# Kernel optimization log

Measured on AMD Instinct MI355X. Metric: run time of the kernel, lower is better.

The kernel has to match this reference:

```python
import jax, jax.numpy as jnp
import numpy as np

RGB2GRAY = jnp.array([0.299, 0.587, 0.114], dtype=jnp.float32)

H_IMG, W_IMG = 1080, 1920
NUM, GRID_Y, GRID_X, GRID_W = 1, 16, 16, 8


def _identity_grids(num, grid_y, grid_x, grid_w):
    ident = jnp.array([1., 0, 0, 0, 0, 1., 0, 0, 0, 0, 1., 0], dtype=jnp.float32)
    return jnp.broadcast_to(ident, (num, grid_y, grid_x, grid_w, 12))


def setup_inputs() -> dict:
    key = jax.random.key(0)
    k1, k2 = jax.random.split(key)
    rgb = jax.random.uniform(k1, (3, H_IMG, W_IMG), dtype=jnp.float32)
    # learned grids = identity affine + small perturbation (so slicing is non-trivial)
    grids = _identity_grids(NUM, GRID_Y, GRID_X, GRID_W) \
        + 0.05 * jax.random.normal(k2, (NUM, GRID_Y, GRID_X, GRID_W, 12), dtype=jnp.float32)
    return {"rgb": rgb, "grids": grids, "idx": 0}


def _bilateral_slice(grid, guidance):
    """Trilinear slice. grid: (Hg, Wg, L, 12); guidance: (Hi, Wi) in [0,1].
    Returns (Hi, Wi, 12)."""
    Hg, Wg, L, _ = grid.shape
    Hi, Wi = guidance.shape
    # align_corners-style pixel -> grid coords
    gy = jnp.linspace(0.0, Hg - 1.0, Hi, dtype=jnp.float32)[:, None]   # (Hi,1)
    gx = jnp.linspace(0.0, Wg - 1.0, Wi, dtype=jnp.float32)[None, :]   # (1,Wi)
    gz = jnp.clip(guidance, 0.0, 1.0) * (L - 1.0)                      # (Hi,Wi)

    fy = jnp.floor(gy); wy = gy - fy
    fx = jnp.floor(gx); wx = gx - fx
    fz = jnp.floor(gz); wz = gz - fz
    y0 = jnp.clip(fy.astype(jnp.int32), 0, Hg - 1); y1 = jnp.clip(y0 + 1, 0, Hg - 1)
    x0 = jnp.clip(fx.astype(jnp.int32), 0, Wg - 1); x1 = jnp.clip(x0 + 1, 0, Wg - 1)
    z0 = jnp.clip(fz.astype(jnp.int32), 0, L - 1);  z1 = jnp.clip(z0 + 1, 0, L - 1)

    out = jnp.zeros((Hi, Wi, 12), dtype=grid.dtype)
    for yi, wyi in ((y0, 1.0 - wy), (y1, wy)):
        for xi, wxi in ((x0, 1.0 - wx), (x1, wx)):
            for zi, wzi in ((z0, 1.0 - wz), (z1, wz)):
                w = (wyi * wxi * wzi)[..., None]          # (Hi,Wi,1)
                out = out + grid[yi, xi, zi] * w          # gather -> (Hi,Wi,12)
    return out


def reference(rgb, grids, idx):
    grid = grids[idx]                         # (Hg, Wg, L, 12)
    rgb_hwc = jnp.transpose(rgb, (1, 2, 0))   # (H, W, 3)
    gray = jnp.tensordot(rgb_hwc, RGB2GRAY, axes=([-1], [0]))  # (H, W)
    affine = _bilateral_slice(grid, gray)     # (H, W, 12)
    affine_mat = affine.reshape(-1, 3, 4)     # (H*W, 3, 4)
    rgb_flat = rgb_hwc.reshape(-1, 3)         # (H*W, 3)
    res_rgb = jnp.einsum('nij,nj->ni', affine_mat[..., :3], rgb_flat) + affine_mat[..., 3]
    return (affine_mat, res_rgb)
```

## Files before the change

kernel.cpp:

```cpp
#include <hip/hip_runtime.h>

#define H_IMG 1080
#define W_IMG 1920
#define HW_PIX (H_IMG * W_IMG)
#define GY 16
#define GX 16
#define GL 8
#define CF 12
#define SEG 192

__global__ __launch_bounds__(192) void bg_kernel(
    const float* __restrict__ rgb,
    const float* __restrict__ grids,
    const int* __restrict__ idxp,
    float* __restrict__ out)
{
    __shared__ float4 sg[96];

    const int tid = threadIdx.x;
    const int y = blockIdx.y;
    const int xbase = blockIdx.x * SEG;

    const float* grid = grids + (size_t)idxp[0] * (GY * GX * GL * CF);

    float gyv = (float)y * (15.0f / 1079.0f);
    float fy = floorf(gyv);
    float wy = gyv - fy;
    int y0 = min(max((int)fy, 0), GY - 1);
    int y1 = min(y0 + 1, GY - 1);

    int xc0 = (int)floorf((float)xbase * (15.0f / 1919.0f));

    if (tid < 96) {
        int xi  = tid / 24;
        int rem = tid - xi * 24;
        int z   = rem / 3;
        int c4  = rem - z * 3;
        int xc  = min(xc0 + xi, GX - 1);
        const float4* c0 = (const float4*)(grid + (size_t)((y0 * GX + xc) * GL + z) * CF) + c4;
        const float4* c1 = (const float4*)(grid + (size_t)((y1 * GX + xc) * GL + z) * CF) + c4;
        float4 a = *c0, b = *c1;
        float wy0 = 1.0f - wy;
        float4 r;
        r.x = wy0 * a.x + wy * b.x;
        r.y = wy0 * a.y + wy * b.y;
        r.z = wy0 * a.z + wy * b.z;
        r.w = wy0 * a.w + wy * b.w;
        sg[tid] = r;
    }
    __syncthreads();

    const int x = xbase + tid;
    const int p = y * W_IMG + x;

    float r = rgb[p];
    float g = rgb[HW_PIX + p];
    float b = rgb[2 * HW_PIX + p];

    float gray = 0.299f * r + 0.587f * g + 0.114f * b;

    float gxv = (float)x * (15.0f / 1919.0f);
    float fx = floorf(gxv), wx = gxv - fx;
    float gz = fminf(fmaxf(gray, 0.0f), 1.0f) * 7.0f;
    float fz = floorf(gz), wz = gz - fz;

    int x0g = min(max((int)fx, 0), GX - 1);
    int x1g = min(x0g + 1, GX - 1);
    int xi0 = x0g - xc0;
    int xi1 = x1g - xc0;
    int z0 = min(max((int)fz, 0), GL - 1);
    int z1 = min(z0 + 1, GL - 1);

    float w00 = (1.0f - wx) * (1.0f - wz);
    float w01 = (1.0f - wx) * wz;
    float w10 = wx * (1.0f - wz);
    float w11 = wx * wz;

    const float4* A = sg + (xi0 * 24 + z0 * 3);
    const float4* B = sg + (xi0 * 24 + z1 * 3);
    const float4* C = sg + (xi1 * 24 + z0 * 3);
    const float4* D = sg + (xi1 * 24 + z1 * 3);

    float4 acc[3];
#pragma unroll
    for (int j = 0; j < 3; ++j) {
        float4 va = A[j], vb = B[j], vc = C[j], vd = D[j];
        float4 o;
        o.x = fmaf(w00, va.x, fmaf(w01, vb.x, fmaf(w10, vc.x, w11 * vd.x)));
        o.y = fmaf(w00, va.y, fmaf(w01, vb.y, fmaf(w10, vc.y, w11 * vd.y)));
        o.z = fmaf(w00, va.z, fmaf(w01, vb.z, fmaf(w10, vc.z, w11 * vd.z)));
        o.w = fmaf(w00, va.w, fmaf(w01, vb.w, fmaf(w10, vc.w, w11 * vd.w)));
        acc[j] = o;
    }

    float4* ao = (float4*)out + (size_t)p * 3;
    ao[0] = acc[0];
    ao[1] = acc[1];
    ao[2] = acc[2];

    float res0 = fmaf(acc[0].x, r, fmaf(acc[0].y, g, fmaf(acc[0].z, b, acc[0].w)));
    float res1 = fmaf(acc[1].x, r, fmaf(acc[1].y, g, fmaf(acc[1].z, b, acc[1].w)));
    float res2 = fmaf(acc[2].x, r, fmaf(acc[2].y, g, fmaf(acc[2].z, b, acc[2].w)));

    float* ro = out + (size_t)HW_PIX * 12 + (size_t)p * 3;
    ro[0] = res0;
    ro[1] = res1;
    ro[2] = res2;
}

extern "C" void kernel_launch(void* const* d_in, const int* in_sizes, int n_in,
                              void* d_out, int out_size, void* d_ws, size_t ws_size,
                              hipStream_t stream) {
    const float* rgb   = (const float*)d_in[0];
    const float* grids = (const float*)d_in[1];
    const int*   idx   = (const int*)d_in[2];
    float*       out   = (float*)d_out;

    dim3 grid(W_IMG / SEG, H_IMG);
    dim3 block(SEG);
    bg_kernel<<<grid, block, 0, stream>>>(rgb, grids, idx, out);
}
```

Before: 154.0 us.

## Assign three threads per pixel so output stores are fully coalesced

Each pixel's work is now split across three threads, one per affine row, with blocks of 128 pixels (384 threads). Consecutive threads write consecutive float4s and consecutive floats, so the stores for both the affine and result outputs become contiguous instead of strided by 3. The trade-off is that the rgb loads and the gray and weight computation are repeated three times per pixel. The shared grid slice also shrinks to three x-cells.

```diff
diff --git a/kernel.cpp b/kernel.cpp
--- a/kernel.cpp
+++ b/kernel.cpp
@@ -7,19 +7,20 @@
 #define GX 16
 #define GL 8
 #define CF 12
-#define SEG 192
+#define PPB 128
+#define TPB (PPB * 3)
 
-__global__ __launch_bounds__(192) void bg_kernel(
+__global__ __launch_bounds__(TPB) void bg_kernel(
     const float* __restrict__ rgb,
     const float* __restrict__ grids,
     const int* __restrict__ idxp,
     float* __restrict__ out)
 {
-    __shared__ float4 sg[96];
+    __shared__ float4 sg[72];
 
     const int tid = threadIdx.x;
     const int y = blockIdx.y;
-    const int xbase = blockIdx.x * SEG;
+    const int xbase = blockIdx.x * PPB;
 
     const float* grid = grids + (size_t)idxp[0] * (GY * GX * GL * CF);
 
@@ -31,7 +32,7 @@
 
     int xc0 = (int)floorf((float)xbase * (15.0f / 1919.0f));
 
-    if (tid < 96) {
+    if (tid < 72) {
         int xi  = tid / 24;
         int rem = tid - xi * 24;
         int z   = rem / 3;
@@ -41,16 +42,18 @@
         const float4* c1 = (const float4*)(grid + (size_t)((y1 * GX + xc) * GL + z) * CF) + c4;
         float4 a = *c0, b = *c1;
         float wy0 = 1.0f - wy;
-        float4 r;
-        r.x = wy0 * a.x + wy * b.x;
-        r.y = wy0 * a.y + wy * b.y;
-        r.z = wy0 * a.z + wy * b.z;
-        r.w = wy0 * a.w + wy * b.w;
-        sg[tid] = r;
+        float4 rr;
+        rr.x = wy0 * a.x + wy * b.x;
+        rr.y = wy0 * a.y + wy * b.y;
+        rr.z = wy0 * a.z + wy * b.z;
+        rr.w = wy0 * a.w + wy * b.w;
+        sg[tid] = rr;
     }
     __syncthreads();
 
-    const int x = xbase + tid;
+    const int k = tid / 3;
+    const int c = tid - k * 3;
+    const int x = xbase + k;
     const int p = y * W_IMG + x;
 
     float r = rgb[p];
@@ -76,36 +79,23 @@
     float w10 = wx * (1.0f - wz);
     float w11 = wx * wz;
 
-    const float4* A = sg + (xi0 * 24 + z0 * 3);
-    const float4* B = sg + (xi0 * 24 + z1 * 3);
-    const float4* C = sg + (xi1 * 24 + z0 * 3);
-    const float4* D = sg + (xi1 * 24 + z1 * 3);
+    float4 A = sg[(xi0 * GL + z0) * 3 + c];
+    float4 B = sg[(xi0 * GL + z1) * 3 + c];
+    float4 C = sg[(xi1 * GL + z0) * 3 + c];
+    float4 D = sg[(xi1 * GL + z1) * 3 + c];
 
-    float4 acc[3];
-#pragma unroll
-    for (int j = 0; j < 3; ++j) {
-        float4 va = A[j], vb = B[j], vc = C[j], vd = D[j];
-        float4 o;
-        o.x = fmaf(w00, va.x, fmaf(w01, vb.x, fmaf(w10, vc.x, w11 * vd.x)));
-        o.y = fmaf(w00, va.y, fmaf(w01, vb.y, fmaf(w10, vc.y, w11 * vd.y)));
-        o.z = fmaf(w00, va.z, fmaf(w01, vb.z, fmaf(w10, vc.z, w11 * vd.z)));
-        o.w = fmaf(w00, va.w, fmaf(w01, vb.w, fmaf(w10, vc.w, w11 * vd.w)));
-        acc[j] = o;
-    }
+    float4 acc;
+    acc.x = fmaf(w00, A.x, fmaf(w01, B.x, fmaf(w10, C.x, w11 * D.x)));
+    acc.y = fmaf(w00, A.y, fmaf(w01, B.y, fmaf(w10, C.y, w11 * D.y)));
+    acc.z = fmaf(w00, A.z, fmaf(w01, B.z, fmaf(w10, C.z, w11 * D.z)));
+    acc.w = fmaf(w00, A.w, fmaf(w01, B.w, fmaf(w10, C.w, w11 * D.w)));
 
-    float4* ao = (float4*)out + (size_t)p * 3;
-    ao[0] = acc[0];
-    ao[1] = acc[1];
-    ao[2] = acc[2];
+    const size_t base3 = (size_t)(y * W_IMG + xbase) * 3;
 
-    float res0 = fmaf(acc[0].x, r, fmaf(acc[0].y, g, fmaf(acc[0].z, b, acc[0].w)));
-    float res1 = fmaf(acc[1].x, r, fmaf(acc[1].y, g, fmaf(acc[1].z, b, acc[1].w)));
-    float res2 = fmaf(acc[2].x, r, fmaf(acc[2].y, g, fmaf(acc[2].z, b, acc[2].w)));
+    ((float4*)out)[base3 + tid] = acc;
 
-    float* ro = out + (size_t)HW_PIX * 12 + (size_t)p * 3;
-    ro[0] = res0;
-    ro[1] = res1;
-    ro[2] = res2;
+    float res = fmaf(acc.x, r, fmaf(acc.y, g, fmaf(acc.z, b, acc.w)));
+    out[(size_t)HW_PIX * 12 + base3 + tid] = res;
 }
 
 extern "C" void kernel_launch(void* const* d_in, const int* in_sizes, int n_in,
@@ -116,7 +106,7 @@
     const int*   idx   = (const int*)d_in[2];
     float*       out   = (float*)d_out;
 
-    dim3 grid(W_IMG / SEG, H_IMG);
-    dim3 block(SEG);
+    dim3 grid(W_IMG / PPB, H_IMG);
+    dim3 block(TPB);
     bg_kernel<<<grid, block, 0, stream>>>(rgb, grids, idx, out);
 }
```

Measured after the change: 158.4 us. 1.03x slower.
